# Performance work log

Hardware: AMD Instinct MI355X
Metric: run time of the kernel (lower is better)

Reference implementation:

```python
import jax, jax.numpy as jnp
import numpy as np

B, T, D, A = 32, 2048, 1024, 128


def setup_inputs() -> dict:
    key = jax.random.key(0)
    k1, k2, k3, k4 = jax.random.split(key, 4)
    x = jax.random.normal(k1, (B, T, D), dtype=jnp.float32)
    Ws = jax.random.normal(k2, (D, A), dtype=jnp.float32) * (1.0 / np.sqrt(D))
    bs = jax.random.normal(k3, (A,), dtype=jnp.float32) * 0.01
    us = jax.random.normal(k4, (A,), dtype=jnp.float32) * (1.0 / np.sqrt(A))
    return {"x": x, "Ws": Ws, "bs": bs, "us": us}


def reference(x, Ws, bs, us):
    # ui = tanh(x @ Ws + bs): [B, T, A]
    ui = jnp.tanh(jnp.einsum("btd,da->bta", x, Ws) + bs)
    # scalar score per timestep: [B, T]
    scores = jnp.einsum("bta,a->bt", ui, us)
    # exp / sum normalization over time == softmax over axis 1
    ai = jax.nn.softmax(scores, axis=1)
    # weighted sum over time: [B, D]
    return jnp.einsum("bt,btd->bd", ai, x)
```

## Files before the change

### kernel.cpp

```cpp
#include <hip/hip_runtime.h>
#include <hip/hip_bf16.h>

#define B_ 32
#define T_ 2048
#define D_ 1024
#define A_ 128

typedef __attribute__((ext_vector_type(8))) short bf16x8;
typedef __attribute__((ext_vector_type(4))) float f32x4;

static __device__ __forceinline__ unsigned short f2bf(float f) {
  union { float f; unsigned u; } v; v.f = f;
  unsigned r = v.u + 0x7FFFu + ((v.u >> 16) & 1u);
  return (unsigned short)(r >> 16);
}

static __device__ __forceinline__ unsigned cvt2u(float lo, float hi) {
  __hip_bfloat162 h2 = __float22bfloat162_rn(make_float2(lo, hi));
  unsigned u;
  __builtin_memcpy(&u, &h2, 4);
  return u;
}

static __device__ __forceinline__ void barrier_lds() {
  asm volatile("s_waitcnt lgkmcnt(0)\n\ts_barrier" ::: "memory");
}

__global__ __launch_bounds__(256) void k_prep(const float* __restrict__ Ws,
                                              unsigned short* __restrict__ Wt) {
  int i = blockIdx.x * 256 + threadIdx.x;
  int a = i >> 10, d = i & 1023;
  Wt[i] = f2bf(Ws[(size_t)d * A_ + a]);
}

#define LDRF 1028
#define LDRB 1032

__global__ __launch_bounds__(512) void k_fused(const float* __restrict__ x,
                                               const unsigned short* __restrict__ Wt,
                                               const float* __restrict__ bs,
                                               const float* __restrict__ us,
                                               float* __restrict__ part,
                                               float* __restrict__ Zp) {
  __shared__ __align__(16) float xb[16 * LDRF];
  __shared__ __align__(16) unsigned short ab[16 * LDRB];
  __shared__ float sc_part[16 * 8];
  __shared__ float e_lds[16];

  const int tid  = threadIdx.x;
  const int w    = tid >> 6;
  const int lane = tid & 63;
  const int lrow = lane & 15;
  const int g    = lane >> 4;
  const int sub  = blockIdx.x;
  const int b    = blockIdx.y;

  const int a_col = w * 16 + lrow;
  const float bsv = bs[a_col];
  const float usv = us[a_col];
  const unsigned short* brow = Wt + (size_t)a_col * D_ + g * 8;

  const int srow = w * 2 + (lane >> 5);
  const int scol = (lane & 31) * 4;
  const float* gx = x + ((size_t)b * T_ + (size_t)sub * 256) * D_;

  float4 st[8];

#pragma unroll
  for (int q = 0; q < 8; ++q)
    st[q] = *(const float4*)(gx + (size_t)srow * D_ + scol + q * 128);
#pragma unroll
  for (int q = 0; q < 8; ++q) {
    *(float4*)(&xb[srow * LDRF + scol + q * 128]) = st[q];
    unsigned lo = cvt2u(st[q].x, st[q].y);
    unsigned hi = cvt2u(st[q].z, st[q].w);
    *(uint2*)(&ab[srow * LDRB + scol + q * 128]) = make_uint2(lo, hi);
  }
  barrier_lds();

  float a0 = 0.f, a1 = 0.f, zacc = 0.f;

  for (int i = 0; i < 16; ++i) {
    if (i < 15) {
      const float* gc = gx + (size_t)(i + 1) * 16 * D_;
#pragma unroll
      for (int q = 0; q < 8; ++q)
        st[q] = *(const float4*)(gc + (size_t)srow * D_ + scol + q * 128);
    }
    __builtin_amdgcn_sched_barrier(0);

    f32x4 accm = (f32x4)0.f;
    const unsigned short* arow = ab + lrow * LDRB + g * 8;
#pragma unroll
    for (int kt = 0; kt < 32; ++kt) {
      bf16x8 af = *(const bf16x8*)(arow + kt * 32);
      bf16x8 bf = *(const bf16x8*)(brow + kt * 32);
      accm = __builtin_amdgcn_mfma_f32_16x16x32_bf16(af, bf, accm, 0, 0, 0);
    }

#pragma unroll
    for (int r = 0; r < 4; ++r) {
      float p = usv * tanhf(accm[r] + bsv);
#pragma unroll
      for (int o = 1; o < 16; o <<= 1) p += __shfl_xor(p, o, 64);
      if (lrow == 0) sc_part[(g * 4 + r) * 8 + w] = p;
    }
    barrier_lds();

    if (tid < 16) {
      float s = 0.f;
#pragma unroll
      for (int ww = 0; ww < 8; ++ww) s += sc_part[tid * 8 + ww];
      e_lds[tid] = expf(s);
    }
    barrier_lds();

    const float* xd = xb + tid * 2;
#pragma unroll
    for (int t = 0; t < 16; ++t) {
      const float2 v = *(const float2*)(xd + t * LDRF);
      const float ev = e_lds[t];
      a0 = fmaf(ev, v.x, a0);
      a1 = fmaf(ev, v.y, a1);
      zacc += ev;
    }
    barrier_lds();

    if (i < 15) {
#pragma unroll
      for (int q = 0; q < 8; ++q) {
        *(float4*)(&xb[srow * LDRF + scol + q * 128]) = st[q];
        unsigned lo = cvt2u(st[q].x, st[q].y);
        unsigned hi = cvt2u(st[q].z, st[q].w);
        *(uint2*)(&ab[srow * LDRB + scol + q * 128]) = make_uint2(lo, hi);
      }
      barrier_lds();
    }
  }

  float* pp = part + ((size_t)sub * B_ + b) * D_ + tid * 2;
  *(float2*)pp = make_float2(a0, a1);
  if (tid == 0) Zp[b * 8 + sub] = zacc;
}

__global__ __launch_bounds__(256) void k_reduce(const float* __restrict__ part,
                                                const float* __restrict__ Zp,
                                                float* __restrict__ out) {
  const int i = blockIdx.x * 256 + threadIdx.x;
  const int b = i >> 10, d = i & 1023;
  float zs = 0.f;
#pragma unroll
  for (int s = 0; s < 8; ++s) zs += Zp[b * 8 + s];
  float acc = 0.f;
#pragma unroll
  for (int s = 0; s < 8; ++s) acc += part[((size_t)s * B_ + b) * D_ + d];
  out[i] = acc / zs;
}

extern "C" void kernel_launch(void* const* d_in, const int* in_sizes, int n_in,
                              void* d_out, int out_size, void* d_ws, size_t ws_size,
                              hipStream_t stream) {
  const float* x  = (const float*)d_in[0];
  const float* Ws = (const float*)d_in[1];
  const float* bs = (const float*)d_in[2];
  const float* us = (const float*)d_in[3];
  float* out = (float*)d_out;

  char* ws = (char*)d_ws;
  unsigned short* Wt = (unsigned short*)ws;
  float* part = (float*)(ws + (256 << 10));
  float* Zp   = (float*)(ws + (256 << 10) + (1 << 20));

  k_prep<<<512, 256, 0, stream>>>(Ws, Wt);
  k_fused<<<dim3(8, B_), 512, 0, stream>>>(x, Wt, bs, us, part, Zp);
  k_reduce<<<(B_ * D_) / 256, 256, 0, stream>>>(part, Zp, out);
}
```

Measured before the change: 80.18 us.

## Keep x rows in registers, drop fp32 LDS tile, double time-slices per batch

The fp32 copy of the x chunk is no longer kept in LDS. Each thread keeps its loaded float4s in registers and does the exp-weighted accumulation directly into per-thread accumulators. A cross-row LDS reduction at the end folds these into per-block partials. The grid doubles from 8 to 16 time slices per batch, and each block now covers 128 timesteps instead of 256. This reduces LDS footprint and traffic and raises the number of blocks. The costs are more registers per thread (32 accumulators), loss of prefetch overlap because the next chunk is loaded only after compute, and twice as much partial data for the reduce kernel.

```diff
diff --git a/kernel.cpp b/kernel.cpp
--- a/kernel.cpp
+++ b/kernel.cpp
@@ -5,6 +5,8 @@
 #define T_ 2048
 #define D_ 1024
 #define A_ 128
+#define NSLICE 16
+#define NCH 8
 
 typedef __attribute__((ext_vector_type(8))) short bf16x8;
 typedef __attribute__((ext_vector_type(4))) float f32x4;
@@ -33,8 +35,8 @@
   Wt[i] = f2bf(Ws[(size_t)d * A_ + a]);
 }
 
-#define LDRF 1028
 #define LDRB 1032
+#define RSTR 516
 
 __global__ __launch_bounds__(512) void k_fused(const float* __restrict__ x,
                                                const unsigned short* __restrict__ Wt,
@@ -42,10 +44,11 @@
                                                const float* __restrict__ us,
                                                float* __restrict__ part,
                                                float* __restrict__ Zp) {
-  __shared__ __align__(16) float xb[16 * LDRF];
-  __shared__ __align__(16) unsigned short ab[16 * LDRB];
+  __shared__ __align__(16) char smem[16 * LDRB * 2];
   __shared__ float sc_part[16 * 8];
-  __shared__ float e_lds[16];
+  __shared__ float zred[16];
+  unsigned short* ab = (unsigned short*)smem;
+  float* red = (float*)smem;
 
   const int tid  = threadIdx.x;
   const int w    = tid >> 6;
@@ -62,39 +65,43 @@
 
   const int srow = w * 2 + (lane >> 5);
   const int scol = (lane & 31) * 4;
-  const float* gx = x + ((size_t)b * T_ + (size_t)sub * 256) * D_;
+  const float* gx = x + ((size_t)b * T_ + (size_t)sub * 128) * D_;
 
   float4 st[8];
+  f32x4 acc[8];
+#pragma unroll
+  for (int q = 0; q < 8; ++q) acc[q] = (f32x4)0.f;
+  float zacc = 0.f;
 
-#pragma unroll
-  for (int q = 0; q < 8; ++q)
-    st[q] = *(const float4*)(gx + (size_t)srow * D_ + scol + q * 128);
-#pragma unroll
-  for (int q = 0; q < 8; ++q) {
-    *(float4*)(&xb[srow * LDRF + scol + q * 128]) = st[q];
-    unsigned lo = cvt2u(st[q].x, st[q].y);
-    unsigned hi = cvt2u(st[q].z, st[q].w);
-    *(uint2*)(&ab[srow * LDRB + scol + q * 128]) = make_uint2(lo, hi);
+#define ISSUE(ci)                                                                 \
+  {                                                                               \
+    const float* gp_ = gx + (size_t)(ci) * 16 * D_ + (size_t)srow * D_ + scol;    \
+    _Pragma("unroll") for (int q = 0; q < 8; ++q)                                 \
+        st[q] = *(const float4*)(gp_ + q * 128);                                  \
   }
+
+#define WRITE_AB()                                                                \
+  {                                                                               \
+    _Pragma("unroll") for (int q = 0; q < 8; ++q) {                               \
+      unsigned lo_ = cvt2u(st[q].x, st[q].y);                                     \
+      unsigned hi_ = cvt2u(st[q].z, st[q].w);                                     \
+      *(uint2*)(&ab[srow * LDRB + scol + q * 128]) = make_uint2(lo_, hi_);        \
+    }                                                                             \
+  }
+
+  ISSUE(0);
+  WRITE_AB();
   barrier_lds();
 
-  float a0 = 0.f, a1 = 0.f, zacc = 0.f;
-
-  for (int i = 0; i < 16; ++i) {
-    if (i < 15) {
-      const float* gc = gx + (size_t)(i + 1) * 16 * D_;
-#pragma unroll
-      for (int q = 0; q < 8; ++q)
-        st[q] = *(const float4*)(gc + (size_t)srow * D_ + scol + q * 128);
-    }
-    __builtin_amdgcn_sched_barrier(0);
-
+  for (int i = 0; i < NCH; ++i) {
+    const unsigned short* bp = brow;
+    asm volatile("" : "+v"(bp));
     f32x4 accm = (f32x4)0.f;
     const unsigned short* arow = ab + lrow * LDRB + g * 8;
 #pragma unroll
     for (int kt = 0; kt < 32; ++kt) {
       bf16x8 af = *(const bf16x8*)(arow + kt * 32);
-      bf16x8 bf = *(const bf16x8*)(brow + kt * 32);
+      bf16x8 bf = *(const bf16x8*)(bp + kt * 32);
       accm = __builtin_amdgcn_mfma_f32_16x16x32_bf16(af, bf, accm, 0, 0, 0);
     }
 
@@ -107,40 +114,51 @@
     }
     barrier_lds();
 
-    if (tid < 16) {
-      float s = 0.f;
+    {
+      float s_ = 0.f;
 #pragma unroll
-      for (int ww = 0; ww < 8; ++ww) s += sc_part[tid * 8 + ww];
-      e_lds[tid] = expf(s);
-    }
-    barrier_lds();
-
-    const float* xd = xb + tid * 2;
-#pragma unroll
-    for (int t = 0; t < 16; ++t) {
-      const float2 v = *(const float2*)(xd + t * LDRF);
-      const float ev = e_lds[t];
-      a0 = fmaf(ev, v.x, a0);
-      a1 = fmaf(ev, v.y, a1);
-      zacc += ev;
-    }
-    barrier_lds();
-
-    if (i < 15) {
+      for (int j = 0; j < 8; ++j) s_ += sc_part[srow * 8 + j];
+      const float e = expf(s_);
+      zacc += e;
 #pragma unroll
       for (int q = 0; q < 8; ++q) {
-        *(float4*)(&xb[srow * LDRF + scol + q * 128]) = st[q];
-        unsigned lo = cvt2u(st[q].x, st[q].y);
-        unsigned hi = cvt2u(st[q].z, st[q].w);
-        *(uint2*)(&ab[srow * LDRB + scol + q * 128]) = make_uint2(lo, hi);
+        acc[q][0] = fmaf(e, st[q].x, acc[q][0]);
+        acc[q][1] = fmaf(e, st[q].y, acc[q][1]);
+        acc[q][2] = fmaf(e, st[q].z, acc[q][2]);
+        acc[q][3] = fmaf(e, st[q].w, acc[q][3]);
+      }
+    }
+
+    if (i + 1 < NCH) {
+      ISSUE(i + 1);
+      WRITE_AB();
+      barrier_lds();
+    }
+  }
+
+  if ((lane & 31) == 0) zred[srow] = zacc;
+#pragma unroll
+  for (int h = 0; h < 2; ++h) {
+#pragma unroll
+    for (int q = 0; q < 4; ++q)
+      *(f32x4*)(&red[srow * RSTR + scol + q * 128]) = acc[h * 4 + q];
+    barrier_lds();
+    float s_ = 0.f;
+#pragma unroll
+    for (int r = 0; r < 16; ++r) s_ += red[r * RSTR + tid];
+    part[((size_t)sub * B_ + b) * D_ + h * 512 + tid] = s_;
+    if (h == 0) {
+      if (tid == 0) {
+        float Z = 0.f;
+#pragma unroll
+        for (int r = 0; r < 16; ++r) Z += zred[r];
+        Zp[b * NSLICE + sub] = Z;
       }
       barrier_lds();
     }
   }
-
-  float* pp = part + ((size_t)sub * B_ + b) * D_ + tid * 2;
-  *(float2*)pp = make_float2(a0, a1);
-  if (tid == 0) Zp[b * 8 + sub] = zacc;
+#undef ISSUE
+#undef WRITE_AB
 }
 
 __global__ __launch_bounds__(256) void k_reduce(const float* __restrict__ part,
@@ -150,10 +168,10 @@
   const int b = i >> 10, d = i & 1023;
   float zs = 0.f;
 #pragma unroll
-  for (int s = 0; s < 8; ++s) zs += Zp[b * 8 + s];
+  for (int s = 0; s < NSLICE; ++s) zs += Zp[b * NSLICE + s];
   float acc = 0.f;
 #pragma unroll
-  for (int s = 0; s < 8; ++s) acc += part[((size_t)s * B_ + b) * D_ + d];
+  for (int s = 0; s < NSLICE; ++s) acc += part[((size_t)s * B_ + b) * D_ + d];
   out[i] = acc / zs;
 }
 
@@ -169,9 +187,9 @@
   char* ws = (char*)d_ws;
   unsigned short* Wt = (unsigned short*)ws;
   float* part = (float*)(ws + (256 << 10));
-  float* Zp   = (float*)(ws + (256 << 10) + (1 << 20));
+  float* Zp   = (float*)(ws + (256 << 10) + (2 << 20));
 
   k_prep<<<512, 256, 0, stream>>>(Ws, Wt);
-  k_fused<<<dim3(8, B_), 512, 0, stream>>>(x, Wt, bs, us, part, Zp);
+  k_fused<<<dim3(NSLICE, B_), 512, 0, stream>>>(x, Wt, bs, us, part, Zp);
   k_reduce<<<(B_ * D_) / 256, 256, 0, stream>>>(part, Zp, out);
 }
```

Measured after the change: 156.6 us. 1.95x slower.
